# Kernel tuning notes

Hardware: AMD Instinct MI355X
Metric: run time of the kernel (lower is better)

Reference implementation:

```python
import jax, jax.numpy as jnp
import numpy as np

N_NODES = 100000
N_EDGES = 800000
IN_DIM = 128
ATT_DIM = 128
N_HEADS = 4
HEAD_DIM = ATT_DIM // N_HEADS


def setup_inputs() -> dict:
    key = jax.random.key(0)
    ks = jax.random.split(key, 10)
    def xavier(k, shape):
        fan_out, fan_in = shape
        lim = jnp.sqrt(6.0 / (fan_in + fan_out))
        return jax.random.uniform(k, shape, jnp.float32, -lim, lim)
    x = jax.random.normal(ks[0], (N_NODES, IN_DIM), jnp.float32)
    edge_index = jax.random.randint(ks[1], (2, N_EDGES), 0, N_NODES, jnp.int64)
    return {
        "x": x,
        "edge_index": edge_index,
        "Wq": xavier(ks[2], (ATT_DIM, IN_DIM)), "bq": jnp.zeros((ATT_DIM,), jnp.float32),
        "Wk": xavier(ks[3], (ATT_DIM, IN_DIM)), "bk": jnp.zeros((ATT_DIM,), jnp.float32),
        "Wv": xavier(ks[4], (ATT_DIM, IN_DIM)), "bv": jnp.zeros((ATT_DIM,), jnp.float32),
        "Wo": xavier(ks[5], (IN_DIM, ATT_DIM)), "bo": jnp.zeros((IN_DIM,), jnp.float32),
    }


def reference(x, edge_index, Wq, bq, Wk, bk, Wv, bv, Wo, bo):
    n = x.shape[0]
    # node projections [N, H, Dh]
    q = (x @ Wq.T + bq).reshape(n, N_HEADS, HEAD_DIM)
    k = (x @ Wk.T + bk).reshape(n, N_HEADS, HEAD_DIM)
    v = (x @ Wv.T + bv).reshape(n, N_HEADS, HEAD_DIM)
    row, col = edge_index[0], edge_index[1]
    # per-edge scores [E, H]
    scores = (q[row] * k[col]).sum(-1) / jnp.sqrt(jnp.float32(HEAD_DIM))
    # segment softmax grouped by destination row
    seg_max = jax.ops.segment_max(scores, row, num_segments=n)  # [N, H]
    e = jnp.exp(scores - seg_max[row])
    seg_sum = jax.ops.segment_sum(e, row, num_segments=n)  # [N, H]
    attn = e / (seg_sum[row] + 1e-16)  # [E, H] (dropout is identity at eval)
    # weighted scatter-add of values
    attended = jax.ops.segment_sum(attn[:, :, None] * v[col], row, num_segments=n)
    attended = attended.reshape(n, ATT_DIM)
    out = attended @ Wo.T + bo + x
    avg_attn = attn.mean(axis=1)  # [E]
    return (out, avg_attn)
```

## Files before the change

### kernel.cpp

```cpp
#include <hip/hip_runtime.h>
#include <hip/hip_bf16.h>

#define DIM 128
#define CAP 64
#define RSQRT_HD 0.17677669529663687f

typedef float f32x4 __attribute__((ext_vector_type(4)));
typedef short bf16x8 __attribute__((ext_vector_type(8)));

__device__ __forceinline__ float bf2f(unsigned short u) {
    unsigned int x = ((unsigned int)u) << 16;
    union { unsigned int i; float f; } c; c.i = x; return c.f;
}
__device__ __forceinline__ unsigned short f2bf(float f) {
    __hip_bfloat16 h = __float2bfloat16(f);
    unsigned short u;
    __builtin_memcpy(&u, &h, 2);
    return u;
}
__device__ __forceinline__ void wave_lds_fence() {
    asm volatile("s_waitcnt lgkmcnt(0)" ::: "memory");
    __builtin_amdgcn_sched_barrier(0);
}

__global__ __launch_bounds__(256) void cast_w4(
    const float* __restrict__ a, const float* __restrict__ b,
    const float* __restrict__ c, const float* __restrict__ d,
    unsigned short* __restrict__ oa, unsigned short* __restrict__ ob,
    unsigned short* __restrict__ oc, unsigned short* __restrict__ od)
{
    int w = blockIdx.y;
    const float* s = (w == 0) ? a : (w == 1) ? b : (w == 2) ? c : d;
    unsigned short* o = (w == 0) ? oa : (w == 1) ? ob : (w == 2) ? oc : od;
    int i = blockIdx.x * 256 + threadIdx.x;
    f32x4 v0 = ((const f32x4*)s)[2 * i];
    f32x4 v1 = ((const f32x4*)s)[2 * i + 1];
    bf16x8 ov;
    ov[0] = (short)f2bf(v0[0]); ov[1] = (short)f2bf(v0[1]);
    ov[2] = (short)f2bf(v0[2]); ov[3] = (short)f2bf(v0[3]);
    ov[4] = (short)f2bf(v1[0]); ov[5] = (short)f2bf(v1[1]);
    ov[6] = (short)f2bf(v1[2]); ov[7] = (short)f2bf(v1[3]);
    ((bf16x8*)o)[i] = ov;
}

__global__ __launch_bounds__(256) void gemm_qkv_fused(const float* __restrict__ X,
    const unsigned short* __restrict__ Wq, const unsigned short* __restrict__ Wk,
    const unsigned short* __restrict__ Wv,
    const float* __restrict__ bq, const float* __restrict__ bk, const float* __restrict__ bv,
    unsigned short* __restrict__ Q, unsigned short* __restrict__ K, unsigned short* __restrict__ V,
    int M)
{
    int lane = threadIdx.x & 63;
    int wave = threadIdx.x >> 6;
    int row0 = blockIdx.x * 128 + wave * 32;
    int r16 = lane & 15;
    int kg = lane >> 4;
    int koff = kg * 8;

    int ra0 = row0 + r16;       if (ra0 > M - 1) ra0 = M - 1;
    int ra1 = row0 + 16 + r16;  if (ra1 > M - 1) ra1 = M - 1;
    const float* pa0f = X + (size_t)ra0 * DIM + koff;
    const float* pa1f = X + (size_t)ra1 * DIM + koff;

    bf16x8 xa0[4], xa1[4];
#pragma unroll
    for (int kt = 0; kt < 4; ++kt) {
        int k0 = kt * 32;
        f32x4 lo0 = *(const f32x4*)(pa0f + k0), hi0 = *(const f32x4*)(pa0f + k0 + 4);
        f32x4 lo1 = *(const f32x4*)(pa1f + k0), hi1 = *(const f32x4*)(pa1f + k0 + 4);
#pragma unroll
        for (int j = 0; j < 4; ++j) {
            xa0[kt][j] = (short)f2bf(lo0[j]); xa0[kt][j + 4] = (short)f2bf(hi0[j]);
            xa1[kt][j] = (short)f2bf(lo1[j]); xa1[kt][j + 4] = (short)f2bf(hi1[j]);
        }
    }

#pragma unroll
    for (int w = 0; w < 3; ++w) {
        const unsigned short* W = (w == 0) ? Wq : (w == 1) ? Wk : Wv;
        const float* bias        = (w == 0) ? bq : (w == 1) ? bk : bv;
        unsigned short* out      = (w == 0) ? Q  : (w == 1) ? K  : V;

        f32x4 acc[2][8] = {};
        const unsigned short* pw = W + r16 * DIM + koff;
#pragma unroll
        for (int kt = 0; kt < 4; ++kt) {
            int k0 = kt * 32;
            bf16x8 bw[8];
#pragma unroll
            for (int ct = 0; ct < 8; ++ct)
                bw[ct] = *(const bf16x8*)(pw + ct * 16 * DIM + k0);
#pragma unroll
            for (int ct = 0; ct < 8; ++ct) {
                acc[0][ct] = __builtin_amdgcn_mfma_f32_16x16x32_bf16(xa0[kt], bw[ct], acc[0][ct], 0, 0, 0);
                acc[1][ct] = __builtin_amdgcn_mfma_f32_16x16x32_bf16(xa1[kt], bw[ct], acc[1][ct], 0, 0, 0);
            }
        }

        float biasv[8];
#pragma unroll
        for (int ct = 0; ct < 8; ++ct) biasv[ct] = bias[ct * 16 + r16];
#pragma unroll
        for (int rt = 0; rt < 2; ++rt) {
            int rbase = row0 + rt * 16 + kg * 4;
#pragma unroll
            for (int ct = 0; ct < 8; ++ct) {
                int c = ct * 16 + r16;
#pragma unroll
                for (int j = 0; j < 4; ++j) {
                    int r = rbase + j;
                    if (r < M) out[(size_t)r * DIM + c] = f2bf(acc[rt][ct][j] + biasv[ct]);
                }
            }
        }
    }
}

__global__ __launch_bounds__(256) void gemm_final(const unsigned short* __restrict__ A,
    const unsigned short* __restrict__ W, const float* __restrict__ bias,
    const float* __restrict__ res, float* __restrict__ out, int M)
{
    int lane = threadIdx.x & 63;
    int wave = threadIdx.x >> 6;
    int row0 = blockIdx.x * 128 + wave * 32;
    int r16 = lane & 15;
    int kg = lane >> 4;
    int koff = kg * 8;

    f32x4 acc[2][8] = {};
    int ra0 = row0 + r16;       if (ra0 > M - 1) ra0 = M - 1;
    int ra1 = row0 + 16 + r16;  if (ra1 > M - 1) ra1 = M - 1;
    const unsigned short* pa0 = A + (size_t)ra0 * DIM + koff;
    const unsigned short* pa1 = A + (size_t)ra1 * DIM + koff;
    const unsigned short* pw = W + r16 * DIM + koff;

#pragma unroll
    for (int k0 = 0; k0 < 128; k0 += 32) {
        bf16x8 a0 = *(const bf16x8*)(pa0 + k0);
        bf16x8 a1 = *(const bf16x8*)(pa1 + k0);
        bf16x8 bw[8];
#pragma unroll
        for (int ct = 0; ct < 8; ++ct)
            bw[ct] = *(const bf16x8*)(pw + ct * 16 * DIM + k0);
#pragma unroll
        for (int ct = 0; ct < 8; ++ct) {
            acc[0][ct] = __builtin_amdgcn_mfma_f32_16x16x32_bf16(a0, bw[ct], acc[0][ct], 0, 0, 0);
            acc[1][ct] = __builtin_amdgcn_mfma_f32_16x16x32_bf16(a1, bw[ct], acc[1][ct], 0, 0, 0);
        }
    }

    float biasv[8];
#pragma unroll
    for (int ct = 0; ct < 8; ++ct) biasv[ct] = bias[ct * 16 + r16];
#pragma unroll
    for (int rt = 0; rt < 2; ++rt) {
        int rbase = row0 + rt * 16 + kg * 4;
#pragma unroll
        for (int ct = 0; ct < 8; ++ct) {
            int c = ct * 16 + r16;
#pragma unroll
            for (int j = 0; j < 4; ++j) {
                int r = rbase + j;
                if (r < M)
                    out[(size_t)r * DIM + c] = acc[rt][ct][j] + biasv[ct] + res[(size_t)r * DIM + c];
            }
        }
    }
}

__global__ void detect64(const int* __restrict__ e, int* __restrict__ flag, int E)
{
    __shared__ int nz;
    int t = threadIdx.x;
    if (t == 0) nz = 0;
    __syncthreads();
    int lim = (E < 4096) ? E : 4096;
    int mynz = 0;
    for (int i = 2 * t + 1; i < lim; i += 512) mynz |= (e[i] != 0);
    if (mynz) atomicOr(&nz, 1);
    __syncthreads();
    if (t == 0) *flag = nz ? 0 : 1;
}

__device__ __forceinline__ int load_idx(const int* p32, const long long* p64, int is64, int i)
{
    return is64 ? (int)p64[i] : p32[i];
}

__global__ void hist_kernel(const int* __restrict__ row32, const long long* __restrict__ row64,
                            const int* __restrict__ flag, int* __restrict__ deg, int E)
{
    int e = blockIdx.x * blockDim.x + threadIdx.x;
    if (e < E) atomicAdd(&deg[load_idx(row32, row64, *flag, e)], 1);
}

__global__ __launch_bounds__(256) void scan1(const int* __restrict__ in, int* __restrict__ incl,
                                             int* __restrict__ bsums, int n)
{
    __shared__ int s[256];
    int t = threadIdx.x;
    int base = blockIdx.x * 1024 + t * 4;
    int v0 = (base + 0 < n) ? in[base + 0] : 0;
    int v1 = (base + 1 < n) ? in[base + 1] : 0;
    int v2 = (base + 2 < n) ? in[base + 2] : 0;
    int v3 = (base + 3 < n) ? in[base + 3] : 0;
    int sum = v0 + v1 + v2 + v3;
    s[t] = sum;
    __syncthreads();
    for (int off = 1; off < 256; off <<= 1) {
        int x = (t >= off) ? s[t - off] : 0;
        __syncthreads();
        s[t] += x;
        __syncthreads();
    }
    int excl = s[t] - sum;
    if (base + 0 < n) incl[base + 0] = excl + v0;
    if (base + 1 < n) incl[base + 1] = excl + v0 + v1;
    if (base + 2 < n) incl[base + 2] = excl + v0 + v1 + v2;
    if (base + 3 < n) incl[base + 3] = excl + sum;
    if (t == 255) bsums[blockIdx.x] = s[255];
}

__global__ __launch_bounds__(256) void scan2(int* bsums, int nb)
{
    __shared__ int s[512];
    int t = threadIdx.x;
    s[t] = (t < nb) ? bsums[t] : 0;
    s[t + 256] = (t + 256 < nb) ? bsums[t + 256] : 0;
    __syncthreads();
    for (int off = 1; off < 512; off <<= 1) {
        int x0 = (t >= off) ? s[t - off] : 0;
        int i1 = t + 256;
        int x1 = (i1 >= off) ? s[i1 - off] : 0;
        __syncthreads();
        s[t] += x0;
        s[i1] += x1;
        __syncthreads();
    }
    if (t < nb) bsums[t] = (t == 0) ? 0 : s[t - 1];
    if (t + 256 < nb) bsums[t + 256] = s[t + 255];
}

__global__ void scan3(const int* __restrict__ incl, const int* __restrict__ bofs,
                      int* __restrict__ rowptr, int n)
{
    int i = blockIdx.x * 256 + threadIdx.x;
    if (i == 0) rowptr[0] = 0;
    if (i < n) rowptr[i + 1] = incl[i] + bofs[i >> 10];
}

__global__ void scatter_kernel(const int* __restrict__ e32, const long long* __restrict__ e64,
                               const int* __restrict__ flag,
                               int* __restrict__ cursor, int* __restrict__ colidx,
                               int* __restrict__ eidb, int E)
{
    int e = blockIdx.x * blockDim.x + threadIdx.x;
    if (e < E) {
        int is64 = *flag;
        int r = load_idx(e32, e64, is64, e);
        int c = load_idx(e32 + E, e64 + E, is64, e);
        int pos = atomicAdd(&cursor[r], 1);
        colidx[pos] = c;
        eidb[pos] = e;
    }
}

__global__ __launch_bounds__(256) void attn_kernel(const unsigned short* __restrict__ Q,
    const unsigned short* __restrict__ K, const unsigned short* __restrict__ V,
    const int* __restrict__ rowptr, const int* __restrict__ colidx,
    const int* __restrict__ eidb, unsigned short* __restrict__ attended,
    float* __restrict__ avg_out, int N)
{
    __shared__ float sc_s[4][CAP * 5];
    __shared__ int scol_s[4][CAP];
    __shared__ int sei_s[4][CAP];

    int wave = threadIdx.x >> 6;
    int l = threadIdx.x & 63;
    int n = blockIdx.x * 4 + wave;
    bool active = n < N;
    int h = l >> 4;
    int hl = l & 15;
    float* sc = sc_s[wave];
    int* scol = scol_s[wave];
    int* sei = sei_s[wave];

    int s0 = active ? rowptr[n] : 0;
    int deg = active ? (rowptr[n + 1] - s0) : 0;

    float q0 = 0.f, q1 = 0.f;
    if (active) {
        ushort2 qq = *(const ushort2*)(Q + (size_t)n * DIM + 2 * l);
        q0 = bf2f(qq.x); q1 = bf2f(qq.y);
    }

    if (deg <= CAP) {
        for (int e = l; e < deg; e += 64) { scol[e] = colidx[s0 + e]; sei[e] = eidb[s0 + e]; }
        wave_lds_fence();
        int e = 0;
        for (; e + 4 <= deg; e += 4) {
            int c0 = scol[e], c1 = scol[e + 1], c2 = scol[e + 2], c3 = scol[e + 3];
            ushort2 k0v = *(const ushort2*)(K + (size_t)c0 * DIM + 2 * l);
            ushort2 k1v = *(const ushort2*)(K + (size_t)c1 * DIM + 2 * l);
            ushort2 k2v = *(const ushort2*)(K + (size_t)c2 * DIM + 2 * l);
            ushort2 k3v = *(const ushort2*)(K + (size_t)c3 * DIM + 2 * l);
            float p0 = q0 * bf2f(k0v.x) + q1 * bf2f(k0v.y);
            float p1 = q0 * bf2f(k1v.x) + q1 * bf2f(k1v.y);
            float p2 = q0 * bf2f(k2v.x) + q1 * bf2f(k2v.y);
            float p3 = q0 * bf2f(k3v.x) + q1 * bf2f(k3v.y);
#pragma unroll
            for (int off = 8; off; off >>= 1) {
                p0 += __shfl_xor(p0, off); p1 += __shfl_xor(p1, off);
                p2 += __shfl_xor(p2, off); p3 += __shfl_xor(p3, off);
            }
            if (hl == 0) {
                sc[(e + 0) * 5 + h] = p0 * RSQRT_HD;
                sc[(e + 1) * 5 + h] = p1 * RSQRT_HD;
                sc[(e + 2) * 5 + h] = p2 * RSQRT_HD;
                sc[(e + 3) * 5 + h] = p3 * RSQRT_HD;
            }
        }
        for (; e < deg; ++e) {
            int c = scol[e];
            ushort2 kk = *(const ushort2*)(K + (size_t)c * DIM + 2 * l);
            float p = q0 * bf2f(kk.x) + q1 * bf2f(kk.y);
#pragma unroll
            for (int off = 8; off; off >>= 1) p += __shfl_xor(p, off);
            if (hl == 0) sc[e * 5 + h] = p * RSQRT_HD;
        }
        wave_lds_fence();
        float m = -INFINITY;
        for (int e2 = hl; e2 < deg; e2 += 16) m = fmaxf(m, sc[e2 * 5 + h]);
#pragma unroll
        for (int off = 8; off; off >>= 1) m = fmaxf(m, __shfl_xor(m, off));
        float ssum = 0.f;
        for (int e2 = hl; e2 < deg; e2 += 16) ssum += __expf(sc[e2 * 5 + h] - m);
#pragma unroll
        for (int off = 8; off; off >>= 1) ssum += __shfl_xor(ssum, off);
        float inv = 1.f / (ssum + 1e-16f);
        for (int e2 = hl; e2 < deg; e2 += 16) sc[e2 * 5 + h] = __expf(sc[e2 * 5 + h] - m) * inv;
        wave_lds_fence();
        for (int e2 = l; e2 < deg; e2 += 64)
            avg_out[sei[e2]] = 0.25f * (sc[e2 * 5] + sc[e2 * 5 + 1] + sc[e2 * 5 + 2] + sc[e2 * 5 + 3]);
        float a0 = 0.f, a1 = 0.f;
        int e3 = 0;
        for (; e3 + 4 <= deg; e3 += 4) {
            int c0 = scol[e3], c1 = scol[e3 + 1], c2 = scol[e3 + 2], c3 = scol[e3 + 3];
            float w0 = sc[(e3 + 0) * 5 + h];
            float w1 = sc[(e3 + 1) * 5 + h];
            float w2 = sc[(e3 + 2) * 5 + h];
            float w3 = sc[(e3 + 3) * 5 + h];
            ushort2 v0 = *(const ushort2*)(V + (size_t)c0 * DIM + 2 * l);
            ushort2 v1 = *(const ushort2*)(V + (size_t)c1 * DIM + 2 * l);
            ushort2 v2 = *(const ushort2*)(V + (size_t)c2 * DIM + 2 * l);
            ushort2 v3 = *(const ushort2*)(V + (size_t)c3 * DIM + 2 * l);
            a0 += w0 * bf2f(v0.x); a1 += w0 * bf2f(v0.y);
            a0 += w1 * bf2f(v1.x); a1 += w1 * bf2f(v1.y);
            a0 += w2 * bf2f(v2.x); a1 += w2 * bf2f(v2.y);
            a0 += w3 * bf2f(v3.x); a1 += w3 * bf2f(v3.y);
        }
        for (; e3 < deg; ++e3) {
            float a = sc[e3 * 5 + h];
            ushort2 vv = *(const ushort2*)(V + (size_t)scol[e3] * DIM + 2 * l);
            a0 += a * bf2f(vv.x);
            a1 += a * bf2f(vv.y);
        }
        if (active) {
            ushort2 o; o.x = f2bf(a0); o.y = f2bf(a1);
            *(ushort2*)(attended + (size_t)n * DIM + 2 * l) = o;
        }
    } else {
        float m = -INFINITY, ssum = 0.f;
        for (int e = 0; e < deg; ++e) {
            int c = colidx[s0 + e];
            ushort2 kk = *(const ushort2*)(K + (size_t)c * DIM + 2 * l);
            float p = q0 * bf2f(kk.x) + q1 * bf2f(kk.y);
#pragma unroll
            for (int off = 8; off; off >>= 1) p += __shfl_xor(p, off);
            p *= RSQRT_HD;
            float mn = fmaxf(m, p);
            ssum = ssum * __expf(m - mn) + __expf(p - mn);
            m = mn;
        }
        float inv = 1.f / (ssum + 1e-16f);
        float a0 = 0.f, a1 = 0.f;
        for (int e = 0; e < deg; ++e) {
            int c = colidx[s0 + e];
            ushort2 kk = *(const ushort2*)(K + (size_t)c * DIM + 2 * l);
            float p = q0 * bf2f(kk.x) + q1 * bf2f(kk.y);
#pragma unroll
            for (int off = 8; off; off >>= 1) p += __shfl_xor(p, off);
            float a = __expf(p * RSQRT_HD - m) * inv;
            float asum = a + __shfl_xor(a, 16);
            asum += __shfl_xor(asum, 32);
            if (l == 0) avg_out[eidb[s0 + e]] = 0.25f * asum;
            ushort2 vv = *(const ushort2*)(V + (size_t)c * DIM + 2 * l);
            a0 += a * bf2f(vv.x);
            a1 += a * bf2f(vv.y);
        }
        if (active) {
            ushort2 o; o.x = f2bf(a0); o.y = f2bf(a1);
            *(ushort2*)(attended + (size_t)n * DIM + 2 * l) = o;
        }
    }
}

extern "C" void kernel_launch(void* const* d_in, const int* in_sizes, int n_in,
                              void* d_out, int out_size, void* d_ws, size_t ws_size,
                              hipStream_t stream)
{
    const float* x  = (const float*)d_in[0];
    const int* e32  = (const int*)d_in[1];
    const long long* e64 = (const long long*)d_in[1];
    const float* Wq = (const float*)d_in[2];
    const float* bq = (const float*)d_in[3];
    const float* Wk = (const float*)d_in[4];
    const float* bk = (const float*)d_in[5];
    const float* Wv = (const float*)d_in[6];
    const float* bv = (const float*)d_in[7];
    const float* Wo = (const float*)d_in[8];
    const float* bo = (const float*)d_in[9];

    int N = in_sizes[0] / DIM;
    int E = in_sizes[1] / 2;

    float* out = (float*)d_out;
    float* avg_out = out + (size_t)N * DIM;

    char* w = (char*)d_ws;
    auto carve = [&](size_t bytes) -> void* {
        void* p = (void*)w;
        w += (bytes + 255) & ~(size_t)255;
        return p;
    };
    unsigned short* Qb = (unsigned short*)carve((size_t)N * DIM * 2);
    unsigned short* Kb = (unsigned short*)carve((size_t)N * DIM * 2);
    unsigned short* Vb = (unsigned short*)carve((size_t)N * DIM * 2);
    unsigned short* Wqb = (unsigned short*)carve(DIM * DIM * 2);
    unsigned short* Wkb = (unsigned short*)carve(DIM * DIM * 2);
    unsigned short* Wvb = (unsigned short*)carve(DIM * DIM * 2);
    unsigned short* Wob = (unsigned short*)carve(DIM * DIM * 2);
    int* deg    = (int*)carve((size_t)N * 4);
    int* tmp    = (int*)carve((size_t)N * 4);
    int* rowptr = (int*)carve(((size_t)N + 1) * 4);
    int* cursor = (int*)carve((size_t)N * 4);
    int* bsums  = (int*)carve(512 * 4);
    int* flag   = (int*)carve(256);
    int* colidx = (int*)carve((size_t)E * 4);
    int* eidb   = (int*)carve((size_t)E * 4);

    hipMemsetAsync(deg, 0, (size_t)N * 4, stream);

    cast_w4<<<dim3(8, 4), 256, 0, stream>>>(Wq, Wk, Wv, Wo, Wqb, Wkb, Wvb, Wob);

    detect64<<<1, 256, 0, stream>>>(e32, flag, 2 * E);
    hist_kernel<<<(E + 255) / 256, 256, 0, stream>>>(e32, e64, flag, deg, E);
    int nb = (N + 1023) / 1024;
    scan1<<<nb, 256, 0, stream>>>(deg, tmp, bsums, N);
    scan2<<<1, 256, 0, stream>>>(bsums, nb);
    scan3<<<(N + 255) / 256, 256, 0, stream>>>(tmp, bsums, rowptr, N);
    hipMemcpyAsync(cursor, rowptr, (size_t)N * 4, hipMemcpyDeviceToDevice, stream);
    scatter_kernel<<<(E + 255) / 256, 256, 0, stream>>>(e32, e64, flag, cursor, colidx, eidb, E);

    int gx = (N + 127) / 128;
    gemm_qkv_fused<<<gx, 256, 0, stream>>>(x, Wqb, Wkb, Wvb, bq, bk, bv, Qb, Kb, Vb, N);

    attn_kernel<<<(N + 3) / 4, 256, 0, stream>>>(Qb, Kb, Vb, rowptr, colidx, eidb,
                                                 Qb , avg_out, N);

    gemm_final<<<gx, 256, 0, stream>>>(Qb, Wob, bo, x, out, N);
}
```

Baseline: 401.1 us.

## Stage QKV stores through LDS, pack col/eid pairs, fuse cursor init into scan

The QKV GEMM epilogue now writes each wave's tile into padded LDS and then emits 16-byte coalesced row stores, replacing scattered 2-byte stores. Column index and edge id are packed into one int2 array, so the scatter does a single 8-byte store and the attention kernel does a single load per edge. The final scan kernel also writes the cursor array (rowptr minus degree), which removes the device-to-device memcpy. The cost is 34 KB of LDS per block in the GEMM, which can limit occupancy.

```diff
diff --git a/kernel.cpp b/kernel.cpp
--- a/kernel.cpp
+++ b/kernel.cpp
@@ -43,138 +43,13 @@
     ((bf16x8*)o)[i] = ov;
 }
 
-__global__ __launch_bounds__(256) void gemm_qkv_fused(const float* __restrict__ X,
-    const unsigned short* __restrict__ Wq, const unsigned short* __restrict__ Wk,
-    const unsigned short* __restrict__ Wv,
-    const float* __restrict__ bq, const float* __restrict__ bk, const float* __restrict__ bv,
-    unsigned short* __restrict__ Q, unsigned short* __restrict__ K, unsigned short* __restrict__ V,
-    int M)
-{
-    int lane = threadIdx.x & 63;
-    int wave = threadIdx.x >> 6;
-    int row0 = blockIdx.x * 128 + wave * 32;
-    int r16 = lane & 15;
-    int kg = lane >> 4;
-    int koff = kg * 8;
-
-    int ra0 = row0 + r16;       if (ra0 > M - 1) ra0 = M - 1;
-    int ra1 = row0 + 16 + r16;  if (ra1 > M - 1) ra1 = M - 1;
-    const float* pa0f = X + (size_t)ra0 * DIM + koff;
-    const float* pa1f = X + (size_t)ra1 * DIM + koff;
-
-    bf16x8 xa0[4], xa1[4];
-#pragma unroll
-    for (int kt = 0; kt < 4; ++kt) {
-        int k0 = kt * 32;
-        f32x4 lo0 = *(const f32x4*)(pa0f + k0), hi0 = *(const f32x4*)(pa0f + k0 + 4);
-        f32x4 lo1 = *(const f32x4*)(pa1f + k0), hi1 = *(const f32x4*)(pa1f + k0 + 4);
-#pragma unroll
-        for (int j = 0; j < 4; ++j) {
-            xa0[kt][j] = (short)f2bf(lo0[j]); xa0[kt][j + 4] = (short)f2bf(hi0[j]);
-            xa1[kt][j] = (short)f2bf(lo1[j]); xa1[kt][j + 4] = (short)f2bf(hi1[j]);
-        }
-    }
-
-#pragma unroll
-    for (int w = 0; w < 3; ++w) {
-        const unsigned short* W = (w == 0) ? Wq : (w == 1) ? Wk : Wv;
-        const float* bias        = (w == 0) ? bq : (w == 1) ? bk : bv;
-        unsigned short* out      = (w == 0) ? Q  : (w == 1) ? K  : V;
-
-        f32x4 acc[2][8] = {};
-        const unsigned short* pw = W + r16 * DIM + koff;
-#pragma unroll
-        for (int kt = 0; kt < 4; ++kt) {
-            int k0 = kt * 32;
-            bf16x8 bw[8];
-#pragma unroll
-            for (int ct = 0; ct < 8; ++ct)
-                bw[ct] = *(const bf16x8*)(pw + ct * 16 * DIM + k0);
-#pragma unroll
-            for (int ct = 0; ct < 8; ++ct) {
-                acc[0][ct] = __builtin_amdgcn_mfma_f32_16x16x32_bf16(xa0[kt], bw[ct], acc[0][ct], 0, 0, 0);
-                acc[1][ct] = __builtin_amdgcn_mfma_f32_16x16x32_bf16(xa1[kt], bw[ct], acc[1][ct], 0, 0, 0);
-            }
-        }
-
-        float biasv[8];
-#pragma unroll
-        for (int ct = 0; ct < 8; ++ct) biasv[ct] = bias[ct * 16 + r16];
-#pragma unroll
-        for (int rt = 0; rt < 2; ++rt) {
-            int rbase = row0 + rt * 16 + kg * 4;
-#pragma unroll
-            for (int ct = 0; ct < 8; ++ct) {
-                int c = ct * 16 + r16;
-#pragma unroll
-                for (int j = 0; j < 4; ++j) {
-                    int r = rbase + j;
-                    if (r < M) out[(size_t)r * DIM + c] = f2bf(acc[rt][ct][j] + biasv[ct]);
-                }
-            }
-        }
-    }
-}
-
-__global__ __launch_bounds__(256) void gemm_final(const unsigned short* __restrict__ A,
-    const unsigned short* __restrict__ W, const float* __restrict__ bias,
-    const float* __restrict__ res, float* __restrict__ out, int M)
-{
-    int lane = threadIdx.x & 63;
-    int wave = threadIdx.x >> 6;
-    int row0 = blockIdx.x * 128 + wave * 32;
-    int r16 = lane & 15;
-    int kg = lane >> 4;
-    int koff = kg * 8;
-
-    f32x4 acc[2][8] = {};
-    int ra0 = row0 + r16;       if (ra0 > M - 1) ra0 = M - 1;
-    int ra1 = row0 + 16 + r16;  if (ra1 > M - 1) ra1 = M - 1;
-    const unsigned short* pa0 = A + (size_t)ra0 * DIM + koff;
-    const unsigned short* pa1 = A + (size_t)ra1 * DIM + koff;
-    const unsigned short* pw = W + r16 * DIM + koff;
-
-#pragma unroll
-    for (int k0 = 0; k0 < 128; k0 += 32) {
-        bf16x8 a0 = *(const bf16x8*)(pa0 + k0);
-        bf16x8 a1 = *(const bf16x8*)(pa1 + k0);
-        bf16x8 bw[8];
-#pragma unroll
-        for (int ct = 0; ct < 8; ++ct)
-            bw[ct] = *(const bf16x8*)(pw + ct * 16 * DIM + k0);
-#pragma unroll
-        for (int ct = 0; ct < 8; ++ct) {
-            acc[0][ct] = __builtin_amdgcn_mfma_f32_16x16x32_bf16(a0, bw[ct], acc[0][ct], 0, 0, 0);
-            acc[1][ct] = __builtin_amdgcn_mfma_f32_16x16x32_bf16(a1, bw[ct], acc[1][ct], 0, 0, 0);
-        }
-    }
-
-    float biasv[8];
-#pragma unroll
-    for (int ct = 0; ct < 8; ++ct) biasv[ct] = bias[ct * 16 + r16];
-#pragma unroll
-    for (int rt = 0; rt < 2; ++rt) {
-        int rbase = row0 + rt * 16 + kg * 4;
-#pragma unroll
-        for (int ct = 0; ct < 8; ++ct) {
-            int c = ct * 16 + r16;
-#pragma unroll
-            for (int j = 0; j < 4; ++j) {
-                int r = rbase + j;
-                if (r < M)
-                    out[(size_t)r * DIM + c] = acc[rt][ct][j] + biasv[ct] + res[(size_t)r * DIM + c];
-            }
-        }
-    }
-}
-
-__global__ void detect64(const int* __restrict__ e, int* __restrict__ flag, int E)
+__global__ void detect64(const int* __restrict__ e, int* __restrict__ flag, int E2)
 {
     __shared__ int nz;
     int t = threadIdx.x;
     if (t == 0) nz = 0;
     __syncthreads();
-    int lim = (E < 4096) ? E : 4096;
+    int lim = (E2 < 4096) ? E2 : 4096;
     int mynz = 0;
     for (int i = 2 * t + 1; i < lim; i += 512) mynz |= (e[i] != 0);
     if (mynz) atomicOr(&nz, 1);
@@ -241,18 +116,22 @@
     if (t + 256 < nb) bsums[t + 256] = s[t + 255];
 }
 
-__global__ void scan3(const int* __restrict__ incl, const int* __restrict__ bofs,
-                      int* __restrict__ rowptr, int n)
+__global__ void scan3c(const int* __restrict__ incl, const int* __restrict__ bofs,
+                       const int* __restrict__ deg, int* __restrict__ rowptr,
+                       int* __restrict__ cursor, int n)
 {
     int i = blockIdx.x * 256 + threadIdx.x;
     if (i == 0) rowptr[0] = 0;
-    if (i < n) rowptr[i + 1] = incl[i] + bofs[i >> 10];
+    if (i < n) {
+        int rp1 = incl[i] + bofs[i >> 10];
+        rowptr[i + 1] = rp1;
+        cursor[i] = rp1 - deg[i];
+    }
 }
 
 __global__ void scatter_kernel(const int* __restrict__ e32, const long long* __restrict__ e64,
                                const int* __restrict__ flag,
-                               int* __restrict__ cursor, int* __restrict__ colidx,
-                               int* __restrict__ eidb, int E)
+                               int* __restrict__ cursor, int2* __restrict__ colEid, int E)
 {
     int e = blockIdx.x * blockDim.x + threadIdx.x;
     if (e < E) {
@@ -260,20 +139,149 @@
         int r = load_idx(e32, e64, is64, e);
         int c = load_idx(e32 + E, e64 + E, is64, e);
         int pos = atomicAdd(&cursor[r], 1);
-        colidx[pos] = c;
-        eidb[pos] = e;
+        colEid[pos] = make_int2(c, e);
+    }
+}
+
+__global__ __launch_bounds__(256) void gemm_qkv_fused(const float* __restrict__ X,
+    const unsigned short* __restrict__ Wq, const unsigned short* __restrict__ Wk,
+    const unsigned short* __restrict__ Wv,
+    const float* __restrict__ bq, const float* __restrict__ bk, const float* __restrict__ bv,
+    unsigned short* __restrict__ Q, unsigned short* __restrict__ K, unsigned short* __restrict__ V,
+    int M)
+{
+    __shared__ unsigned short cst[4][32 * 136];
+    int lane = threadIdx.x & 63;
+    int wave = threadIdx.x >> 6;
+    int row0 = blockIdx.x * 128 + wave * 32;
+    int r16 = lane & 15;
+    int kg = lane >> 4;
+    int koff = kg * 8;
+
+    int ra0 = row0 + r16;       if (ra0 > M - 1) ra0 = M - 1;
+    int ra1 = row0 + 16 + r16;  if (ra1 > M - 1) ra1 = M - 1;
+    const float* pa0f = X + (size_t)ra0 * DIM + koff;
+    const float* pa1f = X + (size_t)ra1 * DIM + koff;
+
+    bf16x8 xa0[4], xa1[4];
+#pragma unroll
+    for (int kt = 0; kt < 4; ++kt) {
+        int k0 = kt * 32;
+        f32x4 lo0 = *(const f32x4*)(pa0f + k0), hi0 = *(const f32x4*)(pa0f + k0 + 4);
+        f32x4 lo1 = *(const f32x4*)(pa1f + k0), hi1 = *(const f32x4*)(pa1f + k0 + 4);
+#pragma unroll
+        for (int j = 0; j < 4; ++j) {
+            xa0[kt][j] = (short)f2bf(lo0[j]); xa0[kt][j + 4] = (short)f2bf(hi0[j]);
+            xa1[kt][j] = (short)f2bf(lo1[j]); xa1[kt][j + 4] = (short)f2bf(hi1[j]);
+        }
+    }
+
+    unsigned short* my = &cst[wave][0];
+#pragma unroll
+    for (int w = 0; w < 3; ++w) {
+        const unsigned short* W = (w == 0) ? Wq : (w == 1) ? Wk : Wv;
+        const float* bias        = (w == 0) ? bq : (w == 1) ? bk : bv;
+        unsigned short* out      = (w == 0) ? Q  : (w == 1) ? K  : V;
+
+        f32x4 acc[2][8] = {};
+        const unsigned short* pw = W + r16 * DIM + koff;
+#pragma unroll
+        for (int kt = 0; kt < 4; ++kt) {
+            int k0 = kt * 32;
+            bf16x8 bw[8];
+#pragma unroll
+            for (int ct = 0; ct < 8; ++ct)
+                bw[ct] = *(const bf16x8*)(pw + ct * 16 * DIM + k0);
+#pragma unroll
+            for (int ct = 0; ct < 8; ++ct) {
+                acc[0][ct] = __builtin_amdgcn_mfma_f32_16x16x32_bf16(xa0[kt], bw[ct], acc[0][ct], 0, 0, 0);
+                acc[1][ct] = __builtin_amdgcn_mfma_f32_16x16x32_bf16(xa1[kt], bw[ct], acc[1][ct], 0, 0, 0);
+            }
+        }
+
+        float biasv[8];
+#pragma unroll
+        for (int ct = 0; ct < 8; ++ct) biasv[ct] = bias[ct * 16 + r16];
+
+#pragma unroll
+        for (int rt = 0; rt < 2; ++rt)
+#pragma unroll
+            for (int ct = 0; ct < 8; ++ct)
+#pragma unroll
+                for (int j = 0; j < 4; ++j)
+                    my[(rt * 16 + kg * 4 + j) * 136 + ct * 16 + r16] =
+                        f2bf(acc[rt][ct][j] + biasv[ct]);
+        wave_lds_fence();
+#pragma unroll
+        for (int pass = 0; pass < 8; ++pass) {
+            int rr = pass * 4 + (lane >> 4);
+            bf16x8 v = *(const bf16x8*)(my + rr * 136 + (lane & 15) * 8);
+            int gr = row0 + rr;
+            if (gr < M) *(bf16x8*)(out + (size_t)gr * DIM + (lane & 15) * 8) = v;
+        }
+        wave_lds_fence();
+    }
+}
+
+__global__ __launch_bounds__(256) void gemm_final(const unsigned short* __restrict__ A,
+    const unsigned short* __restrict__ W, const float* __restrict__ bias,
+    const float* __restrict__ res, float* __restrict__ out, int M)
+{
+    int lane = threadIdx.x & 63;
+    int wave = threadIdx.x >> 6;
+    int row0 = blockIdx.x * 128 + wave * 32;
+    int r16 = lane & 15;
+    int kg = lane >> 4;
+    int koff = kg * 8;
+
+    f32x4 acc[2][8] = {};
+    int ra0 = row0 + r16;       if (ra0 > M - 1) ra0 = M - 1;
+    int ra1 = row0 + 16 + r16;  if (ra1 > M - 1) ra1 = M - 1;
+    const unsigned short* pa0 = A + (size_t)ra0 * DIM + koff;
+    const unsigned short* pa1 = A + (size_t)ra1 * DIM + koff;
+    const unsigned short* pw = W + r16 * DIM + koff;
+
+#pragma unroll
+    for (int k0 = 0; k0 < 128; k0 += 32) {
+        bf16x8 a0 = *(const bf16x8*)(pa0 + k0);
+        bf16x8 a1 = *(const bf16x8*)(pa1 + k0);
+        bf16x8 bw[8];
+#pragma unroll
+        for (int ct = 0; ct < 8; ++ct)
+            bw[ct] = *(const bf16x8*)(pw + ct * 16 * DIM + k0);
+#pragma unroll
+        for (int ct = 0; ct < 8; ++ct) {
+            acc[0][ct] = __builtin_amdgcn_mfma_f32_16x16x32_bf16(a0, bw[ct], acc[0][ct], 0, 0, 0);
+            acc[1][ct] = __builtin_amdgcn_mfma_f32_16x16x32_bf16(a1, bw[ct], acc[1][ct], 0, 0, 0);
+        }
+    }
+
+    float biasv[8];
+#pragma unroll
+    for (int ct = 0; ct < 8; ++ct) biasv[ct] = bias[ct * 16 + r16];
+#pragma unroll
+    for (int rt = 0; rt < 2; ++rt) {
+        int rbase = row0 + rt * 16 + kg * 4;
+#pragma unroll
+        for (int ct = 0; ct < 8; ++ct) {
+            int c = ct * 16 + r16;
+#pragma unroll
+            for (int j = 0; j < 4; ++j) {
+                int r = rbase + j;
+                if (r < M)
+                    out[(size_t)r * DIM + c] = acc[rt][ct][j] + biasv[ct] + res[(size_t)r * DIM + c];
+            }
+        }
     }
 }
 
 __global__ __launch_bounds__(256) void attn_kernel(const unsigned short* __restrict__ Q,
     const unsigned short* __restrict__ K, const unsigned short* __restrict__ V,
-    const int* __restrict__ rowptr, const int* __restrict__ colidx,
-    const int* __restrict__ eidb, unsigned short* __restrict__ attended,
-    float* __restrict__ avg_out, int N)
+    const int* __restrict__ rowptr, const int2* __restrict__ colEid,
+    unsigned short* __restrict__ attended, float* __restrict__ avg_out, int N)
 {
     __shared__ float sc_s[4][CAP * 5];
-    __shared__ int scol_s[4][CAP];
-    __shared__ int sei_s[4][CAP];
+    __shared__ int2 sce_s[4][CAP];
 
     int wave = threadIdx.x >> 6;
     int l = threadIdx.x & 63;
@@ -282,8 +290,7 @@
     int h = l >> 4;
     int hl = l & 15;
     float* sc = sc_s[wave];
-    int* scol = scol_s[wave];
-    int* sei = sei_s[wave];
+    int2* sce = sce_s[wave];
 
     int s0 = active ? rowptr[n] : 0;
     int deg = active ? (rowptr[n + 1] - s0) : 0;
@@ -295,11 +302,11 @@
     }
 
     if (deg <= CAP) {
-        for (int e = l; e < deg; e += 64) { scol[e] = colidx[s0 + e]; sei[e] = eidb[s0 + e]; }
+        for (int e = l; e < deg; e += 64) sce[e] = colEid[s0 + e];
         wave_lds_fence();
         int e = 0;
         for (; e + 4 <= deg; e += 4) {
-            int c0 = scol[e], c1 = scol[e + 1], c2 = scol[e + 2], c3 = scol[e + 3];
+            int c0 = sce[e].x, c1 = sce[e + 1].x, c2 = sce[e + 2].x, c3 = sce[e + 3].x;
             ushort2 k0v = *(const ushort2*)(K + (size_t)c0 * DIM + 2 * l);
             ushort2 k1v = *(const ushort2*)(K + (size_t)c1 * DIM + 2 * l);
             ushort2 k2v = *(const ushort2*)(K + (size_t)c2 * DIM + 2 * l);
@@ -321,7 +328,7 @@
             }
         }
         for (; e < deg; ++e) {
-            int c = scol[e];
+            int c = sce[e].x;
             ushort2 kk = *(const ushort2*)(K + (size_t)c * DIM + 2 * l);
             float p = q0 * bf2f(kk.x) + q1 * bf2f(kk.y);
 #pragma unroll
@@ -341,11 +348,11 @@
         for (int e2 = hl; e2 < deg; e2 += 16) sc[e2 * 5 + h] = __expf(sc[e2 * 5 + h] - m) * inv;
         wave_lds_fence();
         for (int e2 = l; e2 < deg; e2 += 64)
-            avg_out[sei[e2]] = 0.25f * (sc[e2 * 5] + sc[e2 * 5 + 1] + sc[e2 * 5 + 2] + sc[e2 * 5 + 3]);
+            avg_out[sce[e2].y] = 0.25f * (sc[e2 * 5] + sc[e2 * 5 + 1] + sc[e2 * 5 + 2] + sc[e2 * 5 + 3]);
         float a0 = 0.f, a1 = 0.f;
         int e3 = 0;
         for (; e3 + 4 <= deg; e3 += 4) {
-            int c0 = scol[e3], c1 = scol[e3 + 1], c2 = scol[e3 + 2], c3 = scol[e3 + 3];
+            int c0 = sce[e3].x, c1 = sce[e3 + 1].x, c2 = sce[e3 + 2].x, c3 = sce[e3 + 3].x;
             float w0 = sc[(e3 + 0) * 5 + h];
             float w1 = sc[(e3 + 1) * 5 + h];
             float w2 = sc[(e3 + 2) * 5 + h];
@@ -361,7 +368,7 @@
         }
         for (; e3 < deg; ++e3) {
             float a = sc[e3 * 5 + h];
-            ushort2 vv = *(const ushort2*)(V + (size_t)scol[e3] * DIM + 2 * l);
+            ushort2 vv = *(const ushort2*)(V + (size_t)sce[e3].x * DIM + 2 * l);
             a0 += a * bf2f(vv.x);
             a1 += a * bf2f(vv.y);
         }
@@ -372,7 +379,7 @@
     } else {
         float m = -INFINITY, ssum = 0.f;
         for (int e = 0; e < deg; ++e) {
-            int c = colidx[s0 + e];
+            int c = colEid[s0 + e].x;
             ushort2 kk = *(const ushort2*)(K + (size_t)c * DIM + 2 * l);
             float p = q0 * bf2f(kk.x) + q1 * bf2f(kk.y);
 #pragma unroll
@@ -385,16 +392,16 @@
         float inv = 1.f / (ssum + 1e-16f);
         float a0 = 0.f, a1 = 0.f;
         for (int e = 0; e < deg; ++e) {
-            int c = colidx[s0 + e];
-            ushort2 kk = *(const ushort2*)(K + (size_t)c * DIM + 2 * l);
+            int2 ce = colEid[s0 + e];
+            ushort2 kk = *(const ushort2*)(K + (size_t)ce.x * DIM + 2 * l);
             float p = q0 * bf2f(kk.x) + q1 * bf2f(kk.y);
 #pragma unroll
             for (int off = 8; off; off >>= 1) p += __shfl_xor(p, off);
             float a = __expf(p * RSQRT_HD - m) * inv;
             float asum = a + __shfl_xor(a, 16);
             asum += __shfl_xor(asum, 32);
-            if (l == 0) avg_out[eidb[s0 + e]] = 0.25f * asum;
-            ushort2 vv = *(const ushort2*)(V + (size_t)c * DIM + 2 * l);
+            if (l == 0) avg_out[ce.y] = 0.25f * asum;
+            ushort2 vv = *(const ushort2*)(V + (size_t)ce.x * DIM + 2 * l);
             a0 += a * bf2f(vv.x);
             a1 += a * bf2f(vv.y);
         }
@@ -446,8 +453,7 @@
     int* cursor = (int*)carve((size_t)N * 4);
     int* bsums  = (int*)carve(512 * 4);
     int* flag   = (int*)carve(256);
-    int* colidx = (int*)carve((size_t)E * 4);
-    int* eidb   = (int*)carve((size_t)E * 4);
+    int2* colEid = (int2*)carve((size_t)E * 8);
 
     hipMemsetAsync(deg, 0, (size_t)N * 4, stream);
 
@@ -458,14 +464,13 @@
     int nb = (N + 1023) / 1024;
     scan1<<<nb, 256, 0, stream>>>(deg, tmp, bsums, N);
     scan2<<<1, 256, 0, stream>>>(bsums, nb);
-    scan3<<<(N + 255) / 256, 256, 0, stream>>>(tmp, bsums, rowptr, N);
-    hipMemcpyAsync(cursor, rowptr, (size_t)N * 4, hipMemcpyDeviceToDevice, stream);
-    scatter_kernel<<<(E + 255) / 256, 256, 0, stream>>>(e32, e64, flag, cursor, colidx, eidb, E);
+    scan3c<<<(N + 255) / 256, 256, 0, stream>>>(tmp, bsums, deg, rowptr, cursor, N);
+    scatter_kernel<<<(E + 255) / 256, 256, 0, stream>>>(e32, e64, flag, cursor, colEid, E);
 
     int gx = (N + 127) / 128;
     gemm_qkv_fused<<<gx, 256, 0, stream>>>(x, Wqb, Wkb, Wvb, bq, bk, bv, Qb, Kb, Vb, N);
 
-    attn_kernel<<<(N + 3) / 4, 256, 0, stream>>>(Qb, Kb, Vb, rowptr, colidx, eidb,
+    attn_kernel<<<(N + 3) / 4, 256, 0, stream>>>(Qb, Kb, Vb, rowptr, colEid,
                                                  Qb , avg_out, N);
 
     gemm_final<<<gx, 256, 0, stream>>>(Qb, Wob, bo, x, out, N);
```

Result: faster. 386.8 us (-3.6%).
